# Optimization experiments

Hardware: AMD Instinct MI355X
Metric: run time of the kernel (lower is better)

## Reference

```python
import jax, jax.numpy as jnp
import numpy as np

D_MODEL = 1024
NUM_HEADS = 16
HEAD_DIM = D_MODEL // NUM_HEADS
BATCH, SEQ = 4, 4096


def setup_inputs() -> dict:
    key = jax.random.key(0)
    ks = jax.random.split(key, 12)
    std = 0.02
    inp = {
        "query": jax.random.normal(ks[0], (BATCH, SEQ, D_MODEL), dtype=jnp.float32),
        "key": jax.random.normal(ks[1], (BATCH, SEQ, D_MODEL), dtype=jnp.float32),
        "value": jax.random.normal(ks[2], (BATCH, SEQ, D_MODEL), dtype=jnp.float32),
        "mask": jax.random.randint(ks[3], (BATCH, SEQ, 1, 1), 0, 2, dtype=jnp.int32),
        "Wq": jax.random.normal(ks[4], (D_MODEL, D_MODEL), dtype=jnp.float32) * std,
        "bq": jnp.zeros((D_MODEL,), dtype=jnp.float32),
        "Wk": jax.random.normal(ks[5], (D_MODEL, D_MODEL), dtype=jnp.float32) * std,
        "bk": jnp.zeros((D_MODEL,), dtype=jnp.float32),
        "Wv": jax.random.normal(ks[6], (D_MODEL, D_MODEL), dtype=jnp.float32) * std,
        "bv": jnp.zeros((D_MODEL,), dtype=jnp.float32),
        "Wo": jax.random.normal(ks[7], (D_MODEL, D_MODEL), dtype=jnp.float32) * std,
        "bo": jnp.zeros((D_MODEL,), dtype=jnp.float32),
    }
    return inp


def reference(query, key, value, mask, Wq, bq, Wk, bk, Wv, bv, Wo, bo):
    b = query.shape[0]
    # QKV projections (torch nn.Linear: x @ W.T + b)
    Q = query @ Wq.T + bq
    K = key @ Wk.T + bk
    V = value @ Wv.T + bv
    # [b, s, H, hd] -> [b, H, s, hd]
    Q = Q.reshape(b, -1, NUM_HEADS, HEAD_DIM).transpose(0, 2, 1, 3)
    K = K.reshape(b, -1, NUM_HEADS, HEAD_DIM).transpose(0, 2, 1, 3)
    V = V.reshape(b, -1, NUM_HEADS, HEAD_DIM).transpose(0, 2, 1, 3)
    # NOTE: faithful to the original's mislabeled einsum: tensors are [b,H,s,hd]
    # but labels treat axis1 as 'q' and axis2 as 'h', so energy is
    # [batch, seq, heads_q, heads_k] and softmax mixes over heads.
    energy = jnp.einsum('nqhd,nkhd->nhqk', Q, K)
    energy = jnp.where(mask == 0, jnp.float32(-1e20), energy)
    attention = jax.nn.softmax(energy / jnp.sqrt(jnp.float32(D_MODEL)), axis=3)
    # output labeled nqhd -> [b, heads, seq, hd]
    x = jnp.einsum('nhql,nlhd->nqhd', attention, V)
    x = x.transpose(0, 2, 1, 3).reshape(b, -1, D_MODEL)  # [b, s, d_model]
    return x @ Wo.T + bo
```

## Files before the change

kernel.cpp:

```cpp
#include <hip/hip_runtime.h>


typedef unsigned int u32;
typedef unsigned short u16;
typedef __attribute__((ext_vector_type(4))) float f32x4;
typedef __attribute__((ext_vector_type(8))) short bf16x8;

__device__ __forceinline__ void async_copy16(const void* g, void* l) {
  __builtin_amdgcn_global_load_lds(
      (const __attribute__((address_space(1))) void*)g,
      (__attribute__((address_space(3))) void*)l, 16, 0, 0);
}

__device__ __forceinline__ u32 pk_bf16(float a, float b) {
  u32 ua = (__builtin_bit_cast(u32, a) + 0x8000u) >> 16;
  u32 ub = (__builtin_bit_cast(u32, b) + 0x8000u) & 0xFFFF0000u;
  return ua | ub;
}
__device__ __forceinline__ float bflo(u32 u) { return __builtin_bit_cast(float, u << 16); }
__device__ __forceinline__ float bfhi(u32 u) { return __builtin_bit_cast(float, u & 0xFFFF0000u); }

struct F8 { float f[8]; };
__device__ __forceinline__ F8 unp8(uint4 u) {
  F8 r;
  r.f[0] = bflo(u.x); r.f[1] = bfhi(u.x);
  r.f[2] = bflo(u.y); r.f[3] = bfhi(u.y);
  r.f[4] = bflo(u.z); r.f[5] = bfhi(u.z);
  r.f[6] = bflo(u.w); r.f[7] = bfhi(u.w);
  return r;
}

__global__ void cvt_w4(const float* __restrict__ s0, const float* __restrict__ s1,
                       const float* __restrict__ s2, const float* __restrict__ s3,
                       u16* __restrict__ dst) {
  int z = blockIdx.y;
  const float* s = (z == 0) ? s0 : (z == 1) ? s1 : (z == 2) ? s2 : s3;
  u16* d = dst + (size_t)z * (1024 * 1024);
  int i = (blockIdx.x * 256 + threadIdx.x) * 4;
  float4 f = *(const float4*)(s + i);
  uint2 u;
  u.x = pk_bf16(f.x, f.y);
  u.y = pk_bf16(f.z, f.w);
  *(uint2*)(d + i) = u;
}

__global__ void cvt_in3(const float* __restrict__ s0, const float* __restrict__ s1,
                        const float* __restrict__ s2, u16* __restrict__ dst) {
  int z = blockIdx.y;
  const float* s = (z == 0) ? s0 : (z == 1) ? s1 : s2;
  u16* d = dst + (size_t)z * 16777216;
  int i = (blockIdx.x * 256 + threadIdx.x) * 4;
  float4 f = *(const float4*)(s + i);
  uint2 u;
  u.x = pk_bf16(f.x, f.y);
  u.y = pk_bf16(f.z, f.w);
  *(uint2*)(d + i) = u;
}


#define BAR() asm volatile("s_barrier" ::: "memory")
#define VMC(n) asm volatile("s_waitcnt vmcnt(" #n ")" ::: "memory")
#define LGK0() asm volatile("s_waitcnt lgkmcnt(0)" ::: "memory")

template <bool OUTBF>
__device__ __forceinline__ void gemm256_8p(
    const u16* __restrict__ A, const u16* __restrict__ Bm,
    const float* __restrict__ bias, void* __restrict__ Cp,
    int gm0, int gn0, u16* sm) {
  const int tid = threadIdx.x;
  const int lane = tid & 63;
  const int w = tid >> 6;
  const int wm = w >> 2, wn = w & 3;
  const int wr0 = wm * 128, wc0 = wn * 64;
  const int lr = lane & 15, quad = lane >> 4;

  const int sr = tid >> 3;
  const int sc = tid & 7;

  f32x4 acc[8][4];
#pragma unroll
  for (int i = 0; i < 8; i++)
#pragma unroll
    for (int j = 0; j < 4; j++) acc[i][j] = (f32x4){0.f, 0.f, 0.f, 0.f};

  bf16x8 aA[4][2];
  bf16x8 bB[4][2];

#define STAGE_A(buf, h, T) do {                                              \
    int k0_ = ((T) & 15) * 64;                                               \
    u16* lb_ = sm + (buf) * 16384;                                           \
    _Pragma("unroll")                                                        \
    for (int ld_ = 0; ld_ < 2; ld_++) {                                      \
      int row_ = ld_ * 128 + (h) * 64 + sr;       \
      int cs_ = (sc ^ (row_ & 7)) * 8;              \
      async_copy16(A + (size_t)(gm0 + row_) * 1024 + k0_ + cs_,              \
                   lb_ + row_ * 64 + sc * 8);                                \
    }                                                                        \
  } while (0)

#define STAGE_B(buf, bh, T) do {                                             \
    int k0_ = ((T) & 15) * 64;                                               \
    u16* lb_ = sm + 32768 + (buf) * 16384;                                   \
    _Pragma("unroll")                                                        \
    for (int ld_ = 0; ld_ < 2; ld_++) {                                      \
      int ri_ = ld_ * 64 + sr;                                               \
      int row_ = ((ri_ >> 5) << 6) + (bh) * 32 + (ri_ & 31);                 \
      int cs_ = (sc ^ (row_ & 7)) * 8;                                       \
      async_copy16(Bm + (size_t)(gn0 + row_) * 1024 + k0_ + cs_,             \
                   lb_ + row_ * 64 + sc * 8);                                \
    }                                                                        \
  } while (0)

#define READ_A(mh, buf) do {                                                 \
    const u16* lb_ = sm + (buf) * 16384;                                     \
    _Pragma("unroll")                                                        \
    for (int m4_ = 0; m4_ < 4; m4_++)                                        \
      _Pragma("unroll")                                                      \
      for (int kk_ = 0; kk_ < 2; kk_++) {                                    \
        int row_ = wr0 + ((mh) * 4 + m4_) * 16 + lr;                         \
        aA[m4_][kk_] = *(const bf16x8*)(lb_ + row_ * 64 +                    \
                         (((kk_ * 4 + quad) ^ (row_ & 7)) * 8));             \
      }                                                                      \
  } while (0)

#define READ_B(nh, buf) do {                                                 \
    const u16* lb_ = sm + 32768 + (buf) * 16384;                             \
    _Pragma("unroll")                                                        \
    for (int n2_ = 0; n2_ < 2; n2_++)                                        \
      _Pragma("unroll")                                                      \
      for (int kk_ = 0; kk_ < 2; kk_++) {                                    \
        int row_ = wc0 + ((nh) * 2 + n2_) * 16 + lr;                         \
        bB[(nh) * 2 + n2_][kk_] = *(const bf16x8*)(lb_ + row_ * 64 +         \
                         (((kk_ * 4 + quad) ^ (row_ & 7)) * 8));             \
      }                                                                      \
  } while (0)

#define MFMA16(mh, nh) do {                                                  \
    __builtin_amdgcn_s_setprio(1);                                           \
    _Pragma("unroll")                                                        \
    for (int m4_ = 0; m4_ < 4; m4_++)                                        \
      _Pragma("unroll")                                                      \
      for (int n2_ = 0; n2_ < 2; n2_++)                                      \
        _Pragma("unroll")                                                    \
        for (int kk_ = 0; kk_ < 2; kk_++)                                    \
          acc[(mh) * 4 + m4_][(nh) * 2 + n2_] =                              \
              __builtin_amdgcn_mfma_f32_16x16x32_bf16(                       \
                  aA[m4_][kk_], bB[(nh) * 2 + n2_][kk_],                     \
                  acc[(mh) * 4 + m4_][(nh) * 2 + n2_], 0, 0, 0);             \
    __builtin_amdgcn_s_setprio(0);                                           \
  } while (0)

  STAGE_A(0, 0, 0); STAGE_B(0, 0, 0); STAGE_A(0, 1, 0); STAGE_B(0, 1, 0);
  STAGE_A(1, 0, 1); STAGE_B(1, 0, 1); STAGE_A(1, 1, 1);
  VMC(6);
  BAR();

  for (int i = 0; i < 8; i++) {
    const int T1 = 2 * i + 1, T2 = 2 * i + 2, T3 = 2 * i + 3;
    READ_A(0, 0); READ_B(0, 0);
    STAGE_B(1, 1, T1);
    BAR(); MFMA16(0, 0); BAR();
    READ_B(1, 0);
    STAGE_A(0, 0, T2);
    BAR(); MFMA16(0, 1); BAR();
    READ_A(1, 0);
    STAGE_B(0, 0, T2);
    BAR(); MFMA16(1, 0); BAR();
    STAGE_A(0, 1, T2);
    VMC(6);
    BAR(); MFMA16(1, 1); BAR();
    READ_A(0, 1); READ_B(0, 1);
    STAGE_B(0, 1, T2);
    BAR(); MFMA16(0, 0); BAR();
    READ_B(1, 1);
    STAGE_A(1, 0, T3);
    BAR(); MFMA16(0, 1); BAR();
    READ_A(1, 1);
    STAGE_B(1, 0, T3);
    BAR(); MFMA16(1, 0); BAR();
    STAGE_A(1, 1, T3);
    VMC(6);
    BAR(); MFMA16(1, 1); BAR();
  }
  VMC(0);
  BAR();

  if constexpr (OUTBF) {
    float bv[4];
#pragma unroll
    for (int ni = 0; ni < 4; ni++) bv[ni] = bias[gn0 + wc0 + ni * 16 + lr];
#pragma unroll
    for (int mi = 0; mi < 8; mi++)
#pragma unroll
      for (int ni = 0; ni < 4; ni++) {
        int sc_ = wc0 + ((ni ^ quad) << 4) + lr;
#pragma unroll
        for (int r = 0; r < 4; r++) {
          int row = wr0 + mi * 16 + quad * 4 + r;
          float val = acc[mi][ni][r] + bv[ni];
          sm[row * 256 + sc_] = (u16)((__builtin_bit_cast(u32, val) + 0x8000u) >> 16);
        }
      }
    LGK0(); BAR();
    u16* Cg = (u16*)Cp;
#pragma unroll
    for (int j = 0; j < 16; j++) {
      int id = j * 512 + tid;
      int row = id >> 5, ch = id & 31;
      int q = (row >> 2) & 3;
      uint4 vv = *(const uint4*)&sm[row * 256 + ((ch * 8) ^ (q << 4))];
      *(uint4*)&Cg[(size_t)(gm0 + row) * 1024 + gn0 + ch * 8] = vv;
    }
  } else {
    float* cf = (float*)sm;
    float bv[4];
#pragma unroll
    for (int ni = 0; ni < 4; ni++) bv[ni] = bias[gn0 + wc0 + ni * 16 + lr];
#pragma unroll
    for (int h = 0; h < 2; h++) {
#pragma unroll
      for (int m4 = 0; m4 < 4; m4++) {
        int mi = h * 4 + m4;
#pragma unroll
        for (int ni = 0; ni < 4; ni++) {
          int sc_ = wc0 + ((ni ^ quad) << 4) + lr;
#pragma unroll
          for (int r = 0; r < 4; r++) {
            int lrow = (wm << 6) + m4 * 16 + quad * 4 + r;
            cf[lrow * 256 + sc_] = acc[mi][ni][r] + bv[ni];
          }
        }
      }
      LGK0(); BAR();
      float* Cg = (float*)Cp;
#pragma unroll
      for (int j = 0; j < 16; j++) {
        int id = j * 512 + tid;
        int lrow = id >> 6, ch = id & 63;
        int q = (lrow >> 2) & 3;
        float4 vv = *(const float4*)&cf[lrow * 256 + ((ch * 4) ^ (q << 4))];
        int grow = ((lrow >> 6) << 7) + (h << 6) + (lrow & 63);
        *(float4*)&Cg[(size_t)(gm0 + grow) * 1024 + gn0 + ch * 4] = vv;
      }
      if (h == 0) { LGK0(); BAR(); }
    }
  }
#undef STAGE_A
#undef STAGE_B
#undef READ_A
#undef READ_B
#undef MFMA16
}

__global__ __launch_bounds__(512, 2) void gemm_qkv8(
    const u16* __restrict__ X, const u16* __restrict__ W,
    const float* __restrict__ b0, const float* __restrict__ b1,
    const float* __restrict__ b2, u16* __restrict__ out) {
  __shared__ alignas(16) u16 sm[65536];
  const int lin = blockIdx.x;
  const int c = lin & 7;
  const int i = lin >> 3;
  const int z = i >> 5;
  const int r = i & 31;
  const int m = c * 8 + (r >> 2);
  const int n = r & 3;
  const float* bias = (z == 0) ? b0 : (z == 1) ? b1 : b2;
  gemm256_8p<true>(X + (size_t)z * 16777216, W + (size_t)z * 1048576, bias,
                   out + (size_t)z * 16777216, m * 256, n * 256, sm);
}

__global__ __launch_bounds__(512, 2) void gemm_o8(
    const u16* __restrict__ X, const u16* __restrict__ W,
    const float* __restrict__ bias, float* __restrict__ C) {
  __shared__ alignas(16) u16 sm[65536];
  const int lin = blockIdx.x;
  const int c = lin & 7;
  const int i = lin >> 3;
  const int m = c * 8 + (i >> 2);
  const int n = i & 3;
  gemm256_8p<false>(X, W, bias, C, m * 256, n * 256, sm);
}

template <bool AF32, bool OUTBF>
__device__ __forceinline__ void gemm_tile(const void* __restrict__ Ap,
                                          const u16* __restrict__ Bp,
                                          const float* __restrict__ bias,
                                          void* __restrict__ Cp,
                                          int m0, int n0, u16* As, u16* Bs) {
  constexpr int KD = 1024;
  constexpr int ND = 1024;
  const int t = threadIdx.x;
  const int lane = t & 63, w = t >> 6;
  const int wr = (w >> 1) * 64, wc = (w & 1) * 64;
  const int lr = lane & 15, quad = lane >> 4;
  f32x4 acc[4][4] = {};

  for (int k0 = 0; k0 < KD; k0 += 32) {
    __syncthreads();
#pragma unroll
    for (int i = 0; i < 2; i++) {
      int c = i * 256 + t;
      int r = c >> 2, c8 = (c & 3) * 8;
      async_copy16(Bp + ((size_t)(n0 + r) * KD + k0 + c8), &Bs[c * 8]);
    }
    if constexpr (AF32) {
      const float* Af = (const float*)Ap;
      const int r = t >> 2, c8 = (t & 3) * 8;
      const float4* s0 = (const float4*)(Af + (size_t)(m0 + r) * KD + k0 + c8);
      const float4* s1 = (const float4*)(Af + (size_t)(m0 + 64 + r) * KD + k0 + c8);
      float4 f0 = s0[0], f1 = s0[1];
      float4 f2 = s1[0], f3 = s1[1];
      uint4 u0 = { pk_bf16(f0.x, f0.y), pk_bf16(f0.z, f0.w),
                   pk_bf16(f1.x, f1.y), pk_bf16(f1.z, f1.w) };
      uint4 u1 = { pk_bf16(f2.x, f2.y), pk_bf16(f2.z, f2.w),
                   pk_bf16(f3.x, f3.y), pk_bf16(f3.z, f3.w) };
      *(uint4*)&As[t * 8] = u0;
      *(uint4*)&As[(256 + t) * 8] = u1;
    } else {
      const u16* Ab = (const u16*)Ap;
#pragma unroll
      for (int i = 0; i < 2; i++) {
        int c = i * 256 + t;
        int r = c >> 2, c8 = (c & 3) * 8;
        async_copy16(Ab + ((size_t)(m0 + r) * KD + k0 + c8), &As[c * 8]);
      }
    }
    __syncthreads();

    bf16x8 af[4], bfr[4];
#pragma unroll
    for (int mi = 0; mi < 4; mi++)
      af[mi] = *(const bf16x8*)&As[(wr + mi * 16 + lr) * 32 + quad * 8];
#pragma unroll
    for (int ni = 0; ni < 4; ni++)
      bfr[ni] = *(const bf16x8*)&Bs[(wc + ni * 16 + lr) * 32 + quad * 8];
#pragma unroll
    for (int mi = 0; mi < 4; mi++)
#pragma unroll
      for (int ni = 0; ni < 4; ni++)
        acc[mi][ni] = __builtin_amdgcn_mfma_f32_16x16x32_bf16(af[mi], bfr[ni], acc[mi][ni], 0, 0, 0);
  }

#pragma unroll
  for (int ni = 0; ni < 4; ni++) {
    int col = n0 + wc + ni * 16 + lr;
    float bv = bias[col];
#pragma unroll
    for (int mi = 0; mi < 4; mi++) {
      int row = m0 + wr + mi * 16 + quad * 4;
#pragma unroll
      for (int r = 0; r < 4; r++) {
        float val = acc[mi][ni][r] + bv;
        if constexpr (OUTBF) {
          ((u16*)Cp)[(size_t)(row + r) * ND + col] =
              (u16)((__builtin_bit_cast(u32, val) + 0x8000u) >> 16);
        } else {
          ((float*)Cp)[(size_t)(row + r) * ND + col] = val;
        }
      }
    }
  }
}

template <bool AF32>
__global__ __launch_bounds__(256) void gemm_qkv(
    const void* __restrict__ a0, const void* __restrict__ a1, const void* __restrict__ a2,
    const u16* __restrict__ W, const float* __restrict__ b0, const float* __restrict__ b1,
    const float* __restrict__ b2, u16* __restrict__ out) {
  __shared__ alignas(16) u16 As[128 * 32];
  __shared__ alignas(16) u16 Bs[128 * 32];
  const int lin = blockIdx.x;
  const int c = lin & 7;
  const int i = lin >> 3;
  const int z = i >> 7;
  const int r = i & 127;
  const int m = c * 16 + (r >> 3);
  const int n = r & 7;
  const void* A = (z == 0) ? a0 : (z == 1) ? a1 : a2;
  const float* bias = (z == 0) ? b0 : (z == 1) ? b1 : b2;
  gemm_tile<AF32, true>(A, W + (size_t)z * 1048576, bias, out + (size_t)z * 16777216,
                        m * 128, n * 128, As, Bs);
}

__global__ __launch_bounds__(256) void attn_mix(
    const u16* __restrict__ Q, const u16* __restrict__ K,
    const u16* __restrict__ V, const int* __restrict__ mask,
    u16* __restrict__ X) {
  constexpr int RS = 72;
  __shared__ alignas(16) u16 qs[4][16 * RS];
  __shared__ alignas(16) u16 ks[4][16 * RS];
  __shared__ alignas(16) u16 vs[4][16 * RS];

  const int w = threadIdx.x >> 6;
  const int lane = threadIdx.x & 63;
  const int p = blockIdx.x * 4 + w;
  const size_t base = (size_t)p * 1024;

  {
    const uint4* Qg = (const uint4*)(Q + base);
    const uint4* Kg = (const uint4*)(K + base);
    const uint4* Vg = (const uint4*)(V + base);
#pragma unroll
    for (int h = 0; h < 2; h++) {
      int j = h * 64 + lane;
      int off = (j >> 3) * RS + (j & 7) * 8;
      *(uint4*)&qs[w][off] = Qg[j];
      *(uint4*)&ks[w][off] = Kg[j];
      *(uint4*)&vs[w][off] = Vg[j];
    }
  }
  const int mk = mask[p];

  const int qh = lane >> 2, g = lane & 3;
  float e0 = 0.f, e1 = 0.f, e2 = 0.f, e3 = 0.f;
  {
    const u16* qr = &qs[w][qh * RS];
    const u16* k0r = &ks[w][(g * 4 + 0) * RS];
    const u16* k1r = &ks[w][(g * 4 + 1) * RS];
    const u16* k2r = &ks[w][(g * 4 + 2) * RS];
    const u16* k3r = &ks[w][(g * 4 + 3) * RS];
#pragma unroll
    for (int c = 0; c < 8; c++) {
      F8 qf = unp8(*(const uint4*)&qr[c * 8]);
      F8 ka = unp8(*(const uint4*)&k0r[c * 8]);
      F8 kb = unp8(*(const uint4*)&k1r[c * 8]);
      F8 kc = unp8(*(const uint4*)&k2r[c * 8]);
      F8 kd = unp8(*(const uint4*)&k3r[c * 8]);
#pragma unroll
      for (int j = 0; j < 8; j++) {
        e0 += qf.f[j] * ka.f[j];
        e1 += qf.f[j] * kb.f[j];
        e2 += qf.f[j] * kc.f[j];
        e3 += qf.f[j] * kd.f[j];
      }
    }
  }
  const float sc = mk ? 0.03125f : 0.0f;
  float v0 = e0 * sc, v1 = e1 * sc, v2 = e2 * sc, v3 = e3 * sc;
  float mx = fmaxf(fmaxf(v0, v1), fmaxf(v2, v3));
  mx = fmaxf(mx, __shfl_xor(mx, 1, 64));
  mx = fmaxf(mx, __shfl_xor(mx, 2, 64));
  float p0 = __expf(v0 - mx), p1 = __expf(v1 - mx), p2 = __expf(v2 - mx), p3 = __expf(v3 - mx);
  float s = p0 + p1 + p2 + p3;
  s += __shfl_xor(s, 1, 64);
  s += __shfl_xor(s, 2, 64);
  float inv = 1.0f / s;
  float a0 = p0 * inv, a1 = p1 * inv, a2 = p2 * inv, a3 = p3 * inv;

  float xa[16];
#pragma unroll
  for (int i = 0; i < 16; i++) xa[i] = 0.f;
#pragma unroll
  for (int g2 = 0; g2 < 4; g2++) {
    int src = (lane & ~3) | g2;
    float w0 = __shfl(a0, src, 64);
    float w1 = __shfl(a1, src, 64);
    float w2 = __shfl(a2, src, 64);
    float w3 = __shfl(a3, src, 64);
    const float wv[4] = { w0, w1, w2, w3 };
#pragma unroll
    for (int j4 = 0; j4 < 4; j4++) {
      int kh = g2 * 4 + j4;
      float wgt = wv[j4];
      F8 va = unp8(*(const uint4*)&vs[w][kh * RS + g * 16]);
      F8 vb = unp8(*(const uint4*)&vs[w][kh * RS + g * 16 + 8]);
#pragma unroll
      for (int j = 0; j < 8; j++) {
        xa[j] += wgt * va.f[j];
        xa[8 + j] += wgt * vb.f[j];
      }
    }
  }
  uint4 o0 = { pk_bf16(xa[0], xa[1]), pk_bf16(xa[2], xa[3]),
               pk_bf16(xa[4], xa[5]), pk_bf16(xa[6], xa[7]) };
  uint4 o1 = { pk_bf16(xa[8], xa[9]), pk_bf16(xa[10], xa[11]),
               pk_bf16(xa[12], xa[13]), pk_bf16(xa[14], xa[15]) };
  uint4* Xp = (uint4*)(X + base);
  Xp[lane * 2] = o0;
  Xp[lane * 2 + 1] = o1;
}

extern "C" void kernel_launch(void* const* d_in, const int* in_sizes, int n_in,
                              void* d_out, int out_size, void* d_ws, size_t ws_size,
                              hipStream_t stream) {
  const float* q    = (const float*)d_in[0];
  const float* k    = (const float*)d_in[1];
  const float* v    = (const float*)d_in[2];
  const int*   mask = (const int*)d_in[3];
  const float* Wq   = (const float*)d_in[4];
  const float* bq   = (const float*)d_in[5];
  const float* Wk   = (const float*)d_in[6];
  const float* bk   = (const float*)d_in[7];
  const float* Wv   = (const float*)d_in[8];
  const float* bv   = (const float*)d_in[9];
  const float* Wo   = (const float*)d_in[10];
  const float* bo   = (const float*)d_in[11];

  u16* wsb = (u16*)d_ws;
  const bool big = ws_size >= 209715200ull;

  if (big) {
    u16* Wqkv = wsb;
    u16* Wob  = wsb + 3145728;
    u16* qb   = wsb + 4194304;
    u16* Qb   = wsb + 54525952;
    u16* Kb   = Qb + 16777216;
    u16* Vb   = Kb + 16777216;
    u16* Xb   = qb;
    cvt_w4<<<dim3(1024, 4), 256, 0, stream>>>(Wq, Wk, Wv, Wo, wsb);
    cvt_in3<<<dim3(16384, 3), 256, 0, stream>>>(q, k, v, qb);
    gemm_qkv8<<<768, 512, 0, stream>>>(qb, Wqkv, bq, bk, bv, Qb);
    attn_mix<<<4096, 256, 0, stream>>>(Qb, Kb, Vb, mask, Xb);
    gemm_o8<<<256, 512, 0, stream>>>(Xb, Wob, bo, (float*)d_out);
  } else {
    u16* Wqkv = wsb;
    u16* Wob  = wsb + 3145728;
    u16* Qb   = wsb + 4194304;
    u16* Kb   = Qb + 16777216;
    u16* Vb   = Kb + 16777216;
    u16* Xb   = Vb + 16777216;
    cvt_w4<<<dim3(1024, 4), 256, 0, stream>>>(Wq, Wk, Wv, Wo, wsb);
    gemm_qkv<true><<<3072, 256, 0, stream>>>(q, k, v, Wqkv, bq, bk, bv, Qb);
    attn_mix<<<4096, 256, 0, stream>>>(Qb, Kb, Vb, mask, Xb);
    gemm_o8<<<256, 512, 0, stream>>>(Xb, Wob, bo, (float*)d_out);
  }
}
```

Measured before the change: 410.5 us.

## Fuse fp32-to-bf16 input conversion into the pipelined QKV GEMM A-loads

Removes the separate cvt_in3 pass over the three fp32 activation tensors. The QKV GEMM now loads fp32 A tiles into registers, packs them to bf16, and writes them into swizzled LDS, interleaved with the existing async B staging and MFMA phases. This saves a full read of the fp32 inputs, a write and re-read of a bf16 copy, and one kernel launch. In exchange A must go through registers instead of direct global-to-LDS copies, which adds VGPR pressure and conversion ALU inside the GEMM, and the GEMM reads twice as many bytes for A.

```diff
diff --git a/kernel.cpp b/kernel.cpp
--- a/kernel.cpp
+++ b/kernel.cpp
@@ -44,27 +44,14 @@
   *(uint2*)(d + i) = u;
 }
 
-__global__ void cvt_in3(const float* __restrict__ s0, const float* __restrict__ s1,
-                        const float* __restrict__ s2, u16* __restrict__ dst) {
-  int z = blockIdx.y;
-  const float* s = (z == 0) ? s0 : (z == 1) ? s1 : s2;
-  u16* d = dst + (size_t)z * 16777216;
-  int i = (blockIdx.x * 256 + threadIdx.x) * 4;
-  float4 f = *(const float4*)(s + i);
-  uint2 u;
-  u.x = pk_bf16(f.x, f.y);
-  u.y = pk_bf16(f.z, f.w);
-  *(uint2*)(d + i) = u;
-}
-
 
 #define BAR() asm volatile("s_barrier" ::: "memory")
 #define VMC(n) asm volatile("s_waitcnt vmcnt(" #n ")" ::: "memory")
 #define LGK0() asm volatile("s_waitcnt lgkmcnt(0)" ::: "memory")
 
-template <bool OUTBF>
+template <bool OUTBF, bool AFP32>
 __device__ __forceinline__ void gemm256_8p(
-    const u16* __restrict__ A, const u16* __restrict__ Bm,
+    const void* __restrict__ A, const u16* __restrict__ Bm,
     const float* __restrict__ bias, void* __restrict__ Cp,
     int gm0, int gn0, u16* sm) {
   const int tid = threadIdx.x;
@@ -86,16 +73,41 @@
   bf16x8 aA[4][2];
   bf16x8 bB[4][2];
 
+  float4 sA0, sA1, sA2, sA3, sB0, sB1, sB2, sB3;
+
 #define STAGE_A(buf, h, T) do {                                              \
     int k0_ = ((T) & 15) * 64;                                               \
     u16* lb_ = sm + (buf) * 16384;                                           \
+    const u16* Ab_ = (const u16*)A;                                          \
     _Pragma("unroll")                                                        \
     for (int ld_ = 0; ld_ < 2; ld_++) {                                      \
       int row_ = ld_ * 128 + (h) * 64 + sr;       \
       int cs_ = (sc ^ (row_ & 7)) * 8;              \
-      async_copy16(A + (size_t)(gm0 + row_) * 1024 + k0_ + cs_,              \
+      async_copy16(Ab_ + ((size_t)(gm0 + row_) * 1024 + k0_ + cs_),          \
                    lb_ + row_ * 64 + sc * 8);                                \
     }                                                                        \
+  } while (0)
+
+#define AL(v0, v1, v2, v3, h, T) do {                                        \
+    const float* Af_ = (const float*)A;                                      \
+    int k0_ = ((T) & 15) * 64;                                               \
+    int r0_ = (h) * 64 + sr;                                                 \
+    const float* p0_ = Af_ + (size_t)(gm0 + r0_) * 1024 + k0_ + sc * 8;      \
+    const float* p1_ = Af_ + (size_t)(gm0 + 128 + r0_) * 1024 + k0_ + sc * 8;\
+    v0 = *(const float4*)p0_;       v1 = *(const float4*)(p0_ + 4);          \
+    v2 = *(const float4*)p1_;       v3 = *(const float4*)(p1_ + 4);          \
+  } while (0)
+
+#define AW(v0, v1, v2, v3, buf, h) do {                                      \
+    u16* lb_ = sm + (buf) * 16384;                                           \
+    int r0_ = (h) * 64 + sr;                                                 \
+    int cs_ = (sc ^ (sr & 7)) * 8;                                           \
+    uint4 u0_ = { pk_bf16(v0.x, v0.y), pk_bf16(v0.z, v0.w),                  \
+                  pk_bf16(v1.x, v1.y), pk_bf16(v1.z, v1.w) };                \
+    uint4 u1_ = { pk_bf16(v2.x, v2.y), pk_bf16(v2.z, v2.w),                  \
+                  pk_bf16(v3.x, v3.y), pk_bf16(v3.z, v3.w) };                \
+    *(uint4*)&lb_[r0_ * 64 + cs_] = u0_;                                     \
+    *(uint4*)&lb_[(128 + r0_) * 64 + cs_] = u1_;                             \
   } while (0)
 
 #define STAGE_B(buf, bh, T) do {                                             \
@@ -150,10 +162,26 @@
     __builtin_amdgcn_s_setprio(0);                                           \
   } while (0)
 
-  STAGE_A(0, 0, 0); STAGE_B(0, 0, 0); STAGE_A(0, 1, 0); STAGE_B(0, 1, 0);
-  STAGE_A(1, 0, 1); STAGE_B(1, 0, 1); STAGE_A(1, 1, 1);
-  VMC(6);
-  BAR();
+  if constexpr (AFP32) {
+    AL(sA0, sA1, sA2, sA3, 0, 0);
+    AL(sB0, sB1, sB2, sB3, 1, 0);
+    STAGE_B(0, 0, 0); STAGE_B(0, 1, 0);
+    VMC(8);  AW(sA0, sA1, sA2, sA3, 0, 0);
+    AL(sA0, sA1, sA2, sA3, 0, 1);
+    VMC(8);  AW(sB0, sB1, sB2, sB3, 0, 1);
+    AL(sB0, sB1, sB2, sB3, 1, 1);
+    STAGE_B(1, 0, 1);
+    VMC(6);  AW(sA0, sA1, sA2, sA3, 1, 0);
+    AL(sA0, sA1, sA2, sA3, 0, 2);
+    VMC(6);  AW(sB0, sB1, sB2, sB3, 1, 1);
+    LGK0();
+    BAR();
+  } else {
+    STAGE_A(0, 0, 0); STAGE_B(0, 0, 0); STAGE_A(0, 1, 0); STAGE_B(0, 1, 0);
+    STAGE_A(1, 0, 1); STAGE_B(1, 0, 1); STAGE_A(1, 1, 1);
+    VMC(6);
+    BAR();
+  }
 
   for (int i = 0; i < 8; i++) {
     const int T1 = 2 * i + 1, T2 = 2 * i + 2, T3 = 2 * i + 3;
@@ -161,28 +189,53 @@
     STAGE_B(1, 1, T1);
     BAR(); MFMA16(0, 0); BAR();
     READ_B(1, 0);
-    STAGE_A(0, 0, T2);
+    if constexpr (AFP32) {
+      AL(sB0, sB1, sB2, sB3, 1, T2);
+      VMC(6);
+      AW(sA0, sA1, sA2, sA3, 0, 0);
+    } else {
+      STAGE_A(0, 0, T2);
+    }
     BAR(); MFMA16(0, 1); BAR();
     READ_A(1, 0);
     STAGE_B(0, 0, T2);
     BAR(); MFMA16(1, 0); BAR();
-    STAGE_A(0, 1, T2);
-    VMC(6);
+    if constexpr (AFP32) {
+      AL(sA0, sA1, sA2, sA3, 0, T3);
+      VMC(6);
+      AW(sB0, sB1, sB2, sB3, 0, 1);
+    } else {
+      STAGE_A(0, 1, T2);
+      VMC(6);
+    }
     BAR(); MFMA16(1, 1); BAR();
     READ_A(0, 1); READ_B(0, 1);
     STAGE_B(0, 1, T2);
     BAR(); MFMA16(0, 0); BAR();
     READ_B(1, 1);
-    STAGE_A(1, 0, T3);
+    if constexpr (AFP32) {
+      AL(sB0, sB1, sB2, sB3, 1, T3);
+      VMC(6);
+      AW(sA0, sA1, sA2, sA3, 1, 0);
+    } else {
+      STAGE_A(1, 0, T3);
+    }
     BAR(); MFMA16(0, 1); BAR();
     READ_A(1, 1);
     STAGE_B(1, 0, T3);
     BAR(); MFMA16(1, 0); BAR();
-    STAGE_A(1, 1, T3);
-    VMC(6);
+    if constexpr (AFP32) {
+      AL(sA0, sA1, sA2, sA3, 0, T3 + 1);
+      VMC(6);
+      AW(sB0, sB1, sB2, sB3, 1, 1);
+    } else {
+      STAGE_A(1, 1, T3);
+      VMC(6);
+    }
     BAR(); MFMA16(1, 1); BAR();
   }
   VMC(0);
+  LGK0();
   BAR();
 
   if constexpr (OUTBF) {
@@ -250,10 +303,13 @@
 #undef READ_A
 #undef READ_B
 #undef MFMA16
+#undef AL
+#undef AW
 }
 
 __global__ __launch_bounds__(512, 2) void gemm_qkv8(
-    const u16* __restrict__ X, const u16* __restrict__ W,
+    const float* __restrict__ a0, const float* __restrict__ a1,
+    const float* __restrict__ a2, const u16* __restrict__ W,
     const float* __restrict__ b0, const float* __restrict__ b1,
     const float* __restrict__ b2, u16* __restrict__ out) {
   __shared__ alignas(16) u16 sm[65536];
@@ -264,9 +320,10 @@
   const int r = i & 31;
   const int m = c * 8 + (r >> 2);
   const int n = r & 3;
+  const float* A = (z == 0) ? a0 : (z == 1) ? a1 : a2;
   const float* bias = (z == 0) ? b0 : (z == 1) ? b1 : b2;
-  gemm256_8p<true>(X + (size_t)z * 16777216, W + (size_t)z * 1048576, bias,
-                   out + (size_t)z * 16777216, m * 256, n * 256, sm);
+  gemm256_8p<true, true>(A, W + (size_t)z * 1048576, bias,
+                         out + (size_t)z * 16777216, m * 256, n * 256, sm);
 }
 
 __global__ __launch_bounds__(512, 2) void gemm_o8(
@@ -278,7 +335,7 @@
   const int i = lin >> 3;
   const int m = c * 8 + (i >> 2);
   const int n = i & 3;
-  gemm256_8p<false>(X, W, bias, C, m * 256, n * 256, sm);
+  gemm256_8p<false, false>(X, W, bias, C, m * 256, n * 256, sm);
 }
 
 template <bool AF32, bool OUTBF>
@@ -497,29 +554,21 @@
   const float* bo   = (const float*)d_in[11];
 
   u16* wsb = (u16*)d_ws;
-  const bool big = ws_size >= 209715200ull;
-
-  if (big) {
-    u16* Wqkv = wsb;
-    u16* Wob  = wsb + 3145728;
-    u16* qb   = wsb + 4194304;
-    u16* Qb   = wsb + 54525952;
-    u16* Kb   = Qb + 16777216;
-    u16* Vb   = Kb + 16777216;
-    u16* Xb   = qb;
-    cvt_w4<<<dim3(1024, 4), 256, 0, stream>>>(Wq, Wk, Wv, Wo, wsb);
-    cvt_in3<<<dim3(16384, 3), 256, 0, stream>>>(q, k, v, qb);
-    gemm_qkv8<<<768, 512, 0, stream>>>(qb, Wqkv, bq, bk, bv, Qb);
+  const bool ok = ws_size >= 142606336ull;
+
+  u16* Wqkv = wsb;
+  u16* Wob  = wsb + 3145728;
+  u16* Qb   = wsb + 4194304;
+  u16* Kb   = Qb + 16777216;
+  u16* Vb   = Kb + 16777216;
+  u16* Xb   = Vb + 16777216;
+
+  cvt_w4<<<dim3(1024, 4), 256, 0, stream>>>(Wq, Wk, Wv, Wo, wsb);
+  if (ok) {
+    gemm_qkv8<<<768, 512, 0, stream>>>(q, k, v, Wqkv, bq, bk, bv, Qb);
     attn_mix<<<4096, 256, 0, stream>>>(Qb, Kb, Vb, mask, Xb);
     gemm_o8<<<256, 512, 0, stream>>>(Xb, Wob, bo, (float*)d_out);
   } else {
-    u16* Wqkv = wsb;
-    u16* Wob  = wsb + 3145728;
-    u16* Qb   = wsb + 4194304;
-    u16* Kb   = Qb + 16777216;
-    u16* Vb   = Kb + 16777216;
-    u16* Xb   = Vb + 16777216;
-    cvt_w4<<<dim3(1024, 4), 256, 0, stream>>>(Wq, Wk, Wv, Wo, wsb);
     gemm_qkv<true><<<3072, 256, 0, stream>>>(q, k, v, Wqkv, bq, bk, bv, Qb);
     attn_mix<<<4096, 256, 0, stream>>>(Qb, Kb, Vb, mask, Xb);
     gemm_o8<<<256, 512, 0, stream>>>(Xb, Wob, bo, (float*)d_out);
```

Result: slower. 551.3 us (+34.3%).
